# Kernel tuning notes

Hardware: AMD Instinct MI355X
Metric: run time of the kernel (lower is better)

## Reference

```python
import jax, jax.numpy as jnp
import numpy as np

HEAD_DIM = 64
FEAT_H, FEAT_W = 64, 64
ROPE_THETA = 10000.0


def axial_rope_cache(dim, height, width, theta):
    # Matches compute_axial_rope_cache: interleaved cos/sin of shape [H*W, dim]
    theta_dim = (dim // 2) // 2
    freqs = 1.0 / theta ** (jnp.arange(theta_dim, dtype=jnp.float32) * 2.0 / theta_dim)
    t_x = jnp.tile(jnp.arange(width, dtype=jnp.float32)[None, :], (height, 1)).reshape(-1)
    t_y = jnp.tile(jnp.arange(height, dtype=jnp.float32)[:, None], (1, width)).reshape(-1)
    theta_all = jnp.concatenate([jnp.outer(t_x, freqs), jnp.outer(t_y, freqs)], axis=-1)
    cos = jnp.repeat(jnp.cos(theta_all), 2, axis=-1)  # [H*W, dim]
    sin = jnp.repeat(jnp.sin(theta_all), 2, axis=-1)
    return cos, sin


def apply_rope(x, cos, sin):
    # x: [B, H, N, D]; cos/sin: [N, D]
    x1 = x[..., 0::2]
    x2 = x[..., 1::2]
    rot = jnp.stack([-x2, x1], axis=-1).reshape(x.shape)
    return x * cos[None, None] + rot * sin[None, None]


def setup_inputs() -> dict:
    key = jax.random.key(0)
    ks = jax.random.split(key, 11)
    B, Nq, Nk, E, KVD, ID = 1, 4096, 8192, 256, 64, 256
    s_e = 1.0 / np.sqrt(E)
    s_kv = 1.0 / np.sqrt(KVD)
    s_i = 1.0 / np.sqrt(ID)
    return {
        "query": jax.random.normal(ks[0], (B, Nq, E), jnp.float32),
        "key": jax.random.normal(ks[1], (B, Nk, KVD), jnp.float32),
        "value": jax.random.normal(ks[2], (B, Nk, KVD), jnp.float32),
        "Wq": jax.random.normal(ks[3], (E, ID), jnp.float32) * s_e,
        "bq": jnp.zeros((ID,), jnp.float32),
        "Wk": jax.random.normal(ks[4], (KVD, ID), jnp.float32) * s_kv,
        "bk": jnp.zeros((ID,), jnp.float32),
        "Wv": jax.random.normal(ks[5], (KVD, ID), jnp.float32) * s_kv,
        "bv": jnp.zeros((ID,), jnp.float32),
        "Wo": jax.random.normal(ks[6], (ID, E), jnp.float32) * s_i,
        "bo": jnp.zeros((E,), jnp.float32),
        "num_k_exclude_rope": 0,
    }


def reference(query, key, value, Wq, bq, Wk, bk, Wv, bv, Wo, bo, num_k_exclude_rope):
    B, Nq, _ = query.shape
    Nk = key.shape[1]
    H, D = 4, HEAD_DIM

    def split_heads(x):
        b, n, c = x.shape
        return x.reshape(b, n, H, c // H).transpose(0, 2, 1, 3)

    q = split_heads(query @ Wq + bq)  # [B,H,Nq,D]
    k = split_heads(key @ Wk + bk)    # [B,H,Nk,D]
    v = split_heads(value @ Wv + bv)

    cos, sin = axial_rope_cache(D, FEAT_H, FEAT_W, ROPE_THETA)  # [4096, D]
    q = apply_rope(q, cos, sin)

    num_k_rope = Nk - num_k_exclude_rope
    k_spatial = k[:, :, :num_k_rope, :]
    k_other = k[:, :, num_k_rope:, :]
    repeats = num_k_rope // cos.shape[0]  # rope_k_repeat=True
    cos_k = jnp.tile(cos, (repeats, 1))
    sin_k = jnp.tile(sin, (repeats, 1))
    k_spatial = apply_rope(k_spatial, cos_k, sin_k)
    k = jnp.concatenate([k_spatial, k_other], axis=2)

    q = q / jnp.sqrt(jnp.asarray(D, q.dtype))
    scores = jnp.einsum("bhqd,bhkd->bhqk", q, k)
    attn = jax.nn.softmax(scores, axis=-1)
    out = jnp.einsum("bhqk,bhkd->bhqd", attn, v)
    out = out.transpose(0, 2, 1, 3).reshape(B, Nq, H * D)
    return out @ Wo + bo
```

## Files before the change

### kernel.cpp

```cpp
#include <hip/hip_runtime.h>
#include <hip/hip_bf16.h>

#define NQ 4096
#define NK 8192
#define NSPLIT 16
#define KSPAN (NK / NSPLIT)
#define BK 64

#define QSCALE 0.1803368801111204f

typedef short v8s __attribute__((ext_vector_type(8)));
typedef float v4f __attribute__((ext_vector_type(4)));

static __device__ __forceinline__ unsigned short f2bf(float f) {
    unsigned int u = __float_as_uint(f);
    u = (u + 0x7FFFu + ((u >> 16) & 1u)) >> 16;
    return (unsigned short)u;
}
static __device__ __forceinline__ float bf2f(unsigned short h) {
    return __uint_as_float(((unsigned int)h) << 16);
}
static __device__ __forceinline__ unsigned int pkbf(float a, float b) {
    union { __hip_bfloat162 h; unsigned int u; } cv;
    cv.h = __float22bfloat162_rn(make_float2(a, b));
    return cv.u;
}
static __device__ __forceinline__ void split8(const float* a, v8s& hi, v8s& lo) {
#pragma unroll
    for (int j = 0; j < 8; ++j) {
        unsigned short h = f2bf(a[j]);
        hi[j] = (short)h;
        lo[j] = (short)f2bf(a[j] - bf2f(h));
    }
}
static __device__ __forceinline__ void wload(const unsigned short* __restrict__ H,
                                             const unsigned short* __restrict__ L,
                                             int k0, int col, v8s& wh, v8s& wl) {
    const size_t f = (size_t)((k0 >> 3) * 256 + col) * 8;
    wh = *(const v8s*)(H + f);
    wl = *(const v8s*)(L + f);
}
static __device__ __forceinline__ void dma16(const unsigned short* g, unsigned short* l) {
    __builtin_amdgcn_global_load_lds(
        (const __attribute__((address_space(1))) unsigned int*)(const void*)g,
        (__attribute__((address_space(3))) unsigned int*)(void*)l, 16, 0, 0);
}

__global__ __launch_bounds__(256) void prep_kernel(
    const float* __restrict__ Wq, const float* __restrict__ Wk,
    const float* __restrict__ Wv, const float* __restrict__ Wo,
    unsigned short* __restrict__ WqH, unsigned short* __restrict__ WqL,
    unsigned short* __restrict__ WkH, unsigned short* __restrict__ WkL,
    unsigned short* __restrict__ WvH, unsigned short* __restrict__ WvL,
    unsigned short* __restrict__ WoH, unsigned short* __restrict__ WoL)
{
    const int tid = blockIdx.x * 256 + threadIdx.x;
    const float* W;
    unsigned short *H, *L;
    int f;
    if (tid < 8192)        { W = Wq; H = WqH; L = WqL; f = tid; }
    else if (tid < 10240)  { W = Wk; H = WkH; L = WkL; f = tid - 8192; }
    else if (tid < 12288)  { W = Wv; H = WvH; L = WvL; f = tid - 10240; }
    else                   { W = Wo; H = WoH; L = WoL; f = tid - 12288; }
    const int col = f & 255, k0 = (f >> 8) << 3;
    float wv[8];
#pragma unroll
    for (int j = 0; j < 8; ++j) wv[j] = W[(size_t)(k0 + j) * 256 + col];
    v8s hi, lo;
    split8(wv, hi, lo);
    *(v8s*)(H + (size_t)f * 8) = hi;
    *(v8s*)(L + (size_t)f * 8) = lo;
}

__global__ __launch_bounds__(256) void qkv_kernel(
    const float* __restrict__ query, const float* __restrict__ key,
    const float* __restrict__ value,
    const unsigned short* __restrict__ WqH, const unsigned short* __restrict__ WqL,
    const unsigned short* __restrict__ WkH, const unsigned short* __restrict__ WkL,
    const unsigned short* __restrict__ WvH, const unsigned short* __restrict__ WvL,
    const float* __restrict__ bq, const float* __restrict__ bk,
    const float* __restrict__ bv,
    unsigned short* __restrict__ Qb, unsigned short* __restrict__ Kb,
    unsigned short* __restrict__ Vt, const int* __restrict__ nexp)
{
    const int b = blockIdx.x;
    const int t = threadIdx.x, w = t >> 6, lane = t & 63;
    const int quad = lane >> 4, l16 = lane & 15;
    const int colbase = w * 64;

    if (b < 256) {
        const int n0 = b * 16;
        v4f acc[4];
#pragma unroll
        for (int ct = 0; ct < 4; ++ct) {
            const float bb = bq[colbase + ct * 16 + l16];
            acc[ct] = v4f{bb, bb, bb, bb};
        }
        const float* arow = query + (size_t)(n0 + l16) * 256 + quad * 8;
#pragma unroll
        for (int k0 = 0; k0 < 256; k0 += 32) {
            float av[8];
            *(float4*)av = *(const float4*)(arow + k0);
            *(float4*)(av + 4) = *(const float4*)(arow + k0 + 4);
            v8s ah, al;
            split8(av, ah, al);
#pragma unroll
            for (int ct = 0; ct < 4; ++ct) {
                v8s wh, wl;
                wload(WqH, WqL, k0 + quad * 8, colbase + ct * 16 + l16, wh, wl);
                acc[ct] = __builtin_amdgcn_mfma_f32_16x16x32_bf16(al, wh, acc[ct], 0, 0, 0);
                acc[ct] = __builtin_amdgcn_mfma_f32_16x16x32_bf16(ah, wl, acc[ct], 0, 0, 0);
                acc[ct] = __builtin_amdgcn_mfma_f32_16x16x32_bf16(ah, wh, acc[ct], 0, 0, 0);
            }
        }
#pragma unroll
        for (int ct = 0; ct < 4; ++ct) {
            const int d = ct * 16 + l16;
            const int j = d >> 1;
            const float freq = exp2f(-(float)(j & 15) * 1.66096404744368f);
            const bool isx = (j < 16), odd = (d & 1);
#pragma unroll
            for (int r = 0; r < 4; ++r) {
                const int p = n0 + quad * 4 + r;
                const float tpos = isx ? (float)(p & 63) : (float)(p >> 6);
                float sn, cs;
                __sincosf(tpos * freq, &sn, &cs);
                const float x = acc[ct][r];
                const float xp = __shfl_xor(x, 1, 64);
                const float y = odd ? fmaf(x, cs, xp * sn) : fmaf(x, cs, -xp * sn);
                Qb[((size_t)(w * NQ + p) << 6) + d] = f2bf(y * QSCALE);
            }
        }
    } else {
        const bool isK = (b < 768);
        const int n0 = (isK ? (b - 256) : (b - 768)) * 16;
        const float* X = isK ? key : value;
        const unsigned short* WH = isK ? WkH : WvH;
        const unsigned short* WL = isK ? WkL : WvL;
        const float* bias = isK ? bk : bv;
        v4f acc[4];
#pragma unroll
        for (int ct = 0; ct < 4; ++ct) {
            const float bb = bias[colbase + ct * 16 + l16];
            acc[ct] = v4f{bb, bb, bb, bb};
        }
        const float* arow = X + (size_t)(n0 + l16) * 64 + quad * 8;
#pragma unroll
        for (int k0 = 0; k0 < 64; k0 += 32) {
            float av[8];
            *(float4*)av = *(const float4*)(arow + k0);
            *(float4*)(av + 4) = *(const float4*)(arow + k0 + 4);
            v8s ah, al;
            split8(av, ah, al);
#pragma unroll
            for (int ct = 0; ct < 4; ++ct) {
                v8s wh, wl;
                wload(WH, WL, k0 + quad * 8, colbase + ct * 16 + l16, wh, wl);
                acc[ct] = __builtin_amdgcn_mfma_f32_16x16x32_bf16(al, wh, acc[ct], 0, 0, 0);
                acc[ct] = __builtin_amdgcn_mfma_f32_16x16x32_bf16(ah, wl, acc[ct], 0, 0, 0);
                acc[ct] = __builtin_amdgcn_mfma_f32_16x16x32_bf16(ah, wh, acc[ct], 0, 0, 0);
            }
        }
        if (isK) {
            const int nro = NK - *nexp;
#pragma unroll
            for (int ct = 0; ct < 4; ++ct) {
                const int d = ct * 16 + l16;
                const int j = d >> 1;
                const float freq = exp2f(-(float)(j & 15) * 1.66096404744368f);
                const bool isx = (j < 16), odd = (d & 1);
#pragma unroll
                for (int r = 0; r < 4; ++r) {
                    const int p = n0 + quad * 4 + r;
                    const int pc = p & 4095;
                    const float tpos = isx ? (float)(pc & 63) : (float)(pc >> 6);
                    float sn, cs;
                    __sincosf(tpos * freq, &sn, &cs);
                    const float x = acc[ct][r];
                    const float xp = __shfl_xor(x, 1, 64);
                    float y = odd ? fmaf(x, cs, xp * sn) : fmaf(x, cs, -xp * sn);
                    y = (p < nro) ? y : x;
                    Kb[((size_t)(w * NK + p) << 6) + d] = f2bf(y);
                }
            }
        } else {
#pragma unroll
            for (int ct = 0; ct < 4; ++ct) {
                const int col = colbase + ct * 16 + l16;
                uint2 u = make_uint2(pkbf(acc[ct][0], acc[ct][1]),
                                     pkbf(acc[ct][2], acc[ct][3]));
                *(uint2*)(Vt + (size_t)col * NK + n0 + quad * 4) = u;
            }
        }
    }
}

__global__ __launch_bounds__(256) void attn_kernel(
    const unsigned short* __restrict__ Qb, const unsigned short* __restrict__ Kb,
    const unsigned short* __restrict__ Vt, unsigned short* __restrict__ Opart,
    float* __restrict__ Lbuf)
{
    __shared__ alignas(16) unsigned short Kl[2][64 * 64];
    __shared__ alignas(16) unsigned short Vl[2][64 * 64];

    const int blk = blockIdx.x;
    const int s = blk & 15, h = (blk >> 4) & 3, qt = blk >> 6;
    const int t = threadIdx.x;
    const int w = t >> 6, lane = t & 63;
    const int quad = lane >> 4, l16 = lane & 15;

    const int q0 = qt * 128 + w * 32;
    v8s qf[2][2];
#pragma unroll
    for (int g = 0; g < 2; ++g) {
        const unsigned short* qr = Qb + ((size_t)(h * NQ + q0 + g * 16 + l16) << 6) + quad * 8;
        qf[g][0] = *(const v8s*)qr;
        qf[g][1] = *(const v8s*)(qr + 32);
    }

    v4f O[4][2];
#pragma unroll
    for (int dt = 0; dt < 4; ++dt)
#pragma unroll
        for (int g = 0; g < 2; ++g) O[dt][g] = v4f{0.f, 0.f, 0.f, 0.f};
    float psum[2] = {0.f, 0.f};

    const unsigned short* Kbase = Kb + (((size_t)h * NK + s * KSPAN) << 6);
    const unsigned short* Vbase = Vt + (size_t)(h * 64) * NK + s * KSPAN;

    const int srow = lane >> 3;
    const int schunk = (lane & 7) ^ srow;
    const int c0off = ((quad ^ (l16 & 7)) * 8);
    const int c1off = c0off ^ 32;
    int voff[2][2];
#pragma unroll
    for (int tv = 0; tv < 2; ++tv)
#pragma unroll
        for (int h2 = 0; h2 < 2; ++h2)
            voff[tv][h2] = (((4 * tv + 2 * h2 + (quad >> 1)) ^ (l16 & 7)) << 3) + 4 * (quad & 1);

    const int NT = KSPAN / BK;

#pragma unroll
    for (int half = 0; half < 2; ++half) {
        const int r0 = w * 16 + half * 8;
        dma16(Kbase + ((size_t)(r0 + srow) << 6) + schunk * 8, &Kl[0][r0 * 64]);
        dma16(Vbase + (size_t)(r0 + srow) * NK + schunk * 8, &Vl[0][r0 * 64]);
    }

    for (int it = 0; it < NT; ++it) {
        const int cur = it & 1;
        __syncthreads();

        if (it + 1 < NT) {
            const int k1 = (it + 1) * BK;
#pragma unroll
            for (int half = 0; half < 2; ++half) {
                const int r0 = w * 16 + half * 8;
                dma16(Kbase + ((size_t)(k1 + r0 + srow) << 6) + schunk * 8, &Kl[cur ^ 1][r0 * 64]);
                dma16(Vbase + (size_t)(r0 + srow) * NK + k1 + schunk * 8, &Vl[cur ^ 1][r0 * 64]);
            }
        }

        const unsigned short* Klc = &Kl[cur][0];
        const unsigned short* Vlc = &Vl[cur][0];

        v8s pf[2][2];
#pragma unroll
        for (int tt = 0; tt < 4; ++tt) {
            const unsigned short* kr = &Klc[(tt * 16 + l16) * 64];
            const v8s kf0 = *(const v8s*)(kr + c0off);
            const v8s kf1 = *(const v8s*)(kr + c1off);
#pragma unroll
            for (int g = 0; g < 2; ++g) {
                v4f a = v4f{0.f, 0.f, 0.f, 0.f};
                a = __builtin_amdgcn_mfma_f32_16x16x32_bf16(kf0, qf[g][0], a, 0, 0, 0);
                a = __builtin_amdgcn_mfma_f32_16x16x32_bf16(kf1, qf[g][1], a, 0, 0, 0);
                const float e0 = __builtin_amdgcn_exp2f(a[0]);
                const float e1 = __builtin_amdgcn_exp2f(a[1]);
                const float e2 = __builtin_amdgcn_exp2f(a[2]);
                const float e3 = __builtin_amdgcn_exp2f(a[3]);
                psum[g] += (e0 + e1) + (e2 + e3);
                unsigned int* pp = (unsigned int*)&pf[g][tt >> 1];
                pp[(tt & 1) * 2 + 0] = pkbf(e0, e1);
                pp[(tt & 1) * 2 + 1] = pkbf(e2, e3);
            }
        }

#pragma unroll
        for (int dt = 0; dt < 4; ++dt) {
            const unsigned short* vr = &Vlc[(dt * 16 + l16) * 64];
#pragma unroll
            for (int tv = 0; tv < 2; ++tv) {
                union { v8s s; uint2 u[2]; } vv;
                vv.u[0] = *(const uint2*)(vr + voff[tv][0]);
                vv.u[1] = *(const uint2*)(vr + voff[tv][1]);
#pragma unroll
                for (int g = 0; g < 2; ++g)
                    O[dt][g] = __builtin_amdgcn_mfma_f32_16x16x32_bf16(vv.s, pf[g][tv], O[dt][g], 0, 0, 0);
            }
        }
    }

#pragma unroll
    for (int g = 0; g < 2; ++g) {
        float p = psum[g];
        p += __shfl_xor(p, 16, 64);
        p += __shfl_xor(p, 32, 64);
        psum[g] = p;
    }
    unsigned short* Ob = Opart + (size_t)blk * 8192;
#pragma unroll
    for (int g = 0; g < 2; ++g) {
        const int row = w * 32 + g * 16 + l16;
#pragma unroll
        for (int dt = 0; dt < 4; ++dt) {
            uint2 u = make_uint2(pkbf(O[dt][g][0], O[dt][g][1]),
                                 pkbf(O[dt][g][2], O[dt][g][3]));
            *(uint2*)(Ob + row * 64 + dt * 16 + quad * 4) = u;
        }
        if (quad == 0) Lbuf[blk * 128 + row] = psum[g];
    }
}

__global__ __launch_bounds__(512) void oproj_kernel(
    const unsigned short* __restrict__ Opart, const float* __restrict__ Lbuf,
    const unsigned short* __restrict__ WoH, const unsigned short* __restrict__ WoL,
    const float* __restrict__ bo, float* __restrict__ out)
{
    __shared__ alignas(16) unsigned short AH[16][264];
    __shared__ alignas(16) unsigned short AL[16][264];

    const int blk = blockIdx.x;
    const int n0 = blk * 16;
    const int qt = n0 >> 7, rr0 = n0 & 127;
    const int t = threadIdx.x;

    {
        const int row = t >> 5;
        const int d0 = (t & 31) * 8;
        const int h = d0 >> 6, dd0 = d0 & 63;
        const int rr = rr0 + row;
        const int base = qt * 64 + h * 16;
        const unsigned short* op = Opart + (size_t)base * 8192 + rr * 64 + dd0;
        float lsum = 0.f;
        float o[8] = {0.f, 0.f, 0.f, 0.f, 0.f, 0.f, 0.f, 0.f};
#pragma unroll
        for (int s = 0; s < NSPLIT; ++s) {
            lsum += Lbuf[(base + s) * 128 + rr];
            v8s a = *(const v8s*)(op + (size_t)s * 8192);
#pragma unroll
            for (int j = 0; j < 8; ++j) o[j] += bf2f((unsigned short)a[j]);
        }
        const float inv = 1.f / lsum;
#pragma unroll
        for (int j = 0; j < 8; ++j) o[j] *= inv;
        v8s hi, lo;
        split8(o, hi, lo);
        *(v8s*)&AH[row][d0] = hi;
        *(v8s*)&AL[row][d0] = lo;
    }
    __syncthreads();

    const int w = t >> 6, lane = t & 63;
    const int quad = lane >> 4, l16 = lane & 15;
    const int colbase = w * 32;
    v4f acc[2];
#pragma unroll
    for (int ct = 0; ct < 2; ++ct) {
        const float bb = bo[colbase + ct * 16 + l16];
        acc[ct] = v4f{bb, bb, bb, bb};
    }
#pragma unroll
    for (int k0 = 0; k0 < 256; k0 += 32) {
        const v8s ah = *(const v8s*)&AH[l16][k0 + quad * 8];
        const v8s al = *(const v8s*)&AL[l16][k0 + quad * 8];
#pragma unroll
        for (int ct = 0; ct < 2; ++ct) {
            v8s wh, wl;
            wload(WoH, WoL, k0 + quad * 8, colbase + ct * 16 + l16, wh, wl);
            acc[ct] = __builtin_amdgcn_mfma_f32_16x16x32_bf16(al, wh, acc[ct], 0, 0, 0);
            acc[ct] = __builtin_amdgcn_mfma_f32_16x16x32_bf16(ah, wl, acc[ct], 0, 0, 0);
            acc[ct] = __builtin_amdgcn_mfma_f32_16x16x32_bf16(ah, wh, acc[ct], 0, 0, 0);
        }
    }
#pragma unroll
    for (int ct = 0; ct < 2; ++ct)
#pragma unroll
        for (int r = 0; r < 4; ++r)
            out[(size_t)(n0 + quad * 4 + r) * 256 + colbase + ct * 16 + l16] = acc[ct][r];
}

extern "C" void kernel_launch(void* const* d_in, const int* in_sizes, int n_in,
                              void* d_out, int out_size, void* d_ws, size_t ws_size,
                              hipStream_t stream) {
    const float* query = (const float*)d_in[0];
    const float* key   = (const float*)d_in[1];
    const float* value = (const float*)d_in[2];
    const float* Wq    = (const float*)d_in[3];
    const float* bq    = (const float*)d_in[4];
    const float* Wk    = (const float*)d_in[5];
    const float* bk    = (const float*)d_in[6];
    const float* Wv    = (const float*)d_in[7];
    const float* bv    = (const float*)d_in[8];
    const float* Wo    = (const float*)d_in[9];
    const float* bo    = (const float*)d_in[10];
    const int*   nex   = (const int*)d_in[11];

    char* ws = (char*)d_ws;
    const size_t MB = 1024 * 1024;
    unsigned short* Qb    = (unsigned short*)(ws);
    unsigned short* Kb    = (unsigned short*)(ws + 2 * MB);
    unsigned short* Vt    = (unsigned short*)(ws + 6 * MB);
    unsigned short* Opart = (unsigned short*)(ws + 10 * MB);
    float* Lbuf           = (float*)(ws + 42 * MB);
    unsigned short* Wpl   = (unsigned short*)(ws + 43 * MB);
    unsigned short* WqH = Wpl;
    unsigned short* WqL = Wpl + 65536;
    unsigned short* WkH = Wpl + 131072;
    unsigned short* WkL = Wpl + 147456;
    unsigned short* WvH = Wpl + 163840;
    unsigned short* WvL = Wpl + 180224;
    unsigned short* WoH = Wpl + 196608;
    unsigned short* WoL = Wpl + 262144;
    float* out = (float*)d_out;

    prep_kernel<<<80, 256, 0, stream>>>(Wq, Wk, Wv, Wo,
                                        WqH, WqL, WkH, WkL, WvH, WvL, WoH, WoL);
    qkv_kernel<<<1280, 256, 0, stream>>>(query, key, value,
                                         WqH, WqL, WkH, WkL, WvH, WvL,
                                         bq, bk, bv, Qb, Kb, Vt, nex);
    attn_kernel<<<2048, 256, 0, stream>>>(Qb, Kb, Vt, Opart, Lbuf);
    oproj_kernel<<<256, 512, 0, stream>>>(Opart, Lbuf, WoH, WoL, bo, out);
}
```

Baseline: 155.2 us.

## Drop LDS staging in attention, load K/V fragments from global; halve split count

The attention kernel no longer double-buffers K and V tiles into LDS with async global-to-LDS copies and barriers. Each lane now reads its MFMA K and V fragments straight from global memory, relying on L1/L2 caching across the four waves that share them. The key-split count is also halved from 16 to 8, so there are fewer blocks doing longer loops, fewer partial outputs, and a smaller reduction in oproj. The trade is no more barriers and no LDS use, but repeated uncoalesced global reads per wave and less latency hiding with half the blocks.

```diff
diff --git a/kernel.cpp b/kernel.cpp
--- a/kernel.cpp
+++ b/kernel.cpp
@@ -3,7 +3,7 @@
 
 #define NQ 4096
 #define NK 8192
-#define NSPLIT 16
+#define NSPLIT 8
 #define KSPAN (NK / NSPLIT)
 #define BK 64
 
@@ -39,11 +39,6 @@
     const size_t f = (size_t)((k0 >> 3) * 256 + col) * 8;
     wh = *(const v8s*)(H + f);
     wl = *(const v8s*)(L + f);
-}
-static __device__ __forceinline__ void dma16(const unsigned short* g, unsigned short* l) {
-    __builtin_amdgcn_global_load_lds(
-        (const __attribute__((address_space(1))) unsigned int*)(const void*)g,
-        (__attribute__((address_space(3))) unsigned int*)(void*)l, 16, 0, 0);
 }
 
 __global__ __launch_bounds__(256) void prep_kernel(
@@ -200,11 +195,8 @@
     const unsigned short* __restrict__ Vt, unsigned short* __restrict__ Opart,
     float* __restrict__ Lbuf)
 {
-    __shared__ alignas(16) unsigned short Kl[2][64 * 64];
-    __shared__ alignas(16) unsigned short Vl[2][64 * 64];
-
     const int blk = blockIdx.x;
-    const int s = blk & 15, h = (blk >> 4) & 3, qt = blk >> 6;
+    const int s = blk & 7, h = (blk >> 3) & 3, qt = blk >> 5;
     const int t = threadIdx.x;
     const int w = t >> 6, lane = t & 63;
     const int quad = lane >> 4, l16 = lane & 15;
@@ -225,52 +217,16 @@
         for (int g = 0; g < 2; ++g) O[dt][g] = v4f{0.f, 0.f, 0.f, 0.f};
     float psum[2] = {0.f, 0.f};
 
-    const unsigned short* Kbase = Kb + (((size_t)h * NK + s * KSPAN) << 6);
-    const unsigned short* Vbase = Vt + (size_t)(h * 64) * NK + s * KSPAN;
-
-    const int srow = lane >> 3;
-    const int schunk = (lane & 7) ^ srow;
-    const int c0off = ((quad ^ (l16 & 7)) * 8);
-    const int c1off = c0off ^ 32;
-    int voff[2][2];
-#pragma unroll
-    for (int tv = 0; tv < 2; ++tv)
-#pragma unroll
-        for (int h2 = 0; h2 < 2; ++h2)
-            voff[tv][h2] = (((4 * tv + 2 * h2 + (quad >> 1)) ^ (l16 & 7)) << 3) + 4 * (quad & 1);
-
-    const int NT = KSPAN / BK;
-
-#pragma unroll
-    for (int half = 0; half < 2; ++half) {
-        const int r0 = w * 16 + half * 8;
-        dma16(Kbase + ((size_t)(r0 + srow) << 6) + schunk * 8, &Kl[0][r0 * 64]);
-        dma16(Vbase + (size_t)(r0 + srow) * NK + schunk * 8, &Vl[0][r0 * 64]);
-    }
-
-    for (int it = 0; it < NT; ++it) {
-        const int cur = it & 1;
-        __syncthreads();
-
-        if (it + 1 < NT) {
-            const int k1 = (it + 1) * BK;
-#pragma unroll
-            for (int half = 0; half < 2; ++half) {
-                const int r0 = w * 16 + half * 8;
-                dma16(Kbase + ((size_t)(k1 + r0 + srow) << 6) + schunk * 8, &Kl[cur ^ 1][r0 * 64]);
-                dma16(Vbase + (size_t)(r0 + srow) * NK + k1 + schunk * 8, &Vl[cur ^ 1][r0 * 64]);
-            }
-        }
-
-        const unsigned short* Klc = &Kl[cur][0];
-        const unsigned short* Vlc = &Vl[cur][0];
-
+    const unsigned short* Krow = Kb + (((size_t)h * NK + s * KSPAN + l16) << 6) + quad * 8;
+    const unsigned short* Vrow = Vt + (size_t)(h * 64 + l16) * NK + s * KSPAN + quad * 4;
+
+    for (int k0 = 0; k0 < KSPAN; k0 += BK) {
         v8s pf[2][2];
 #pragma unroll
         for (int tt = 0; tt < 4; ++tt) {
-            const unsigned short* kr = &Klc[(tt * 16 + l16) * 64];
-            const v8s kf0 = *(const v8s*)(kr + c0off);
-            const v8s kf1 = *(const v8s*)(kr + c1off);
+            const unsigned short* kr = Krow + ((size_t)(k0 + tt * 16) << 6);
+            const v8s kf0 = *(const v8s*)kr;
+            const v8s kf1 = *(const v8s*)(kr + 32);
 #pragma unroll
             for (int g = 0; g < 2; ++g) {
                 v4f a = v4f{0.f, 0.f, 0.f, 0.f};
@@ -289,12 +245,12 @@
 
 #pragma unroll
         for (int dt = 0; dt < 4; ++dt) {
-            const unsigned short* vr = &Vlc[(dt * 16 + l16) * 64];
+            const unsigned short* vr = Vrow + (size_t)(dt * 16) * NK + k0;
 #pragma unroll
             for (int tv = 0; tv < 2; ++tv) {
                 union { v8s s; uint2 u[2]; } vv;
-                vv.u[0] = *(const uint2*)(vr + voff[tv][0]);
-                vv.u[1] = *(const uint2*)(vr + voff[tv][1]);
+                vv.u[0] = *(const uint2*)(vr + tv * 32);
+                vv.u[1] = *(const uint2*)(vr + tv * 32 + 16);
 #pragma unroll
                 for (int g = 0; g < 2; ++g)
                     O[dt][g] = __builtin_amdgcn_mfma_f32_16x16x32_bf16(vv.s, pf[g][tv], O[dt][g], 0, 0, 0);
@@ -341,7 +297,7 @@
         const int d0 = (t & 31) * 8;
         const int h = d0 >> 6, dd0 = d0 & 63;
         const int rr = rr0 + row;
-        const int base = qt * 64 + h * 16;
+        const int base = qt * 32 + h * 8;
         const unsigned short* op = Opart + (size_t)base * 8192 + rr * 64 + dd0;
         float lsum = 0.f;
         float o[8] = {0.f, 0.f, 0.f, 0.f, 0.f, 0.f, 0.f, 0.f};
@@ -413,8 +369,8 @@
     unsigned short* Kb    = (unsigned short*)(ws + 2 * MB);
     unsigned short* Vt    = (unsigned short*)(ws + 6 * MB);
     unsigned short* Opart = (unsigned short*)(ws + 10 * MB);
-    float* Lbuf           = (float*)(ws + 42 * MB);
-    unsigned short* Wpl   = (unsigned short*)(ws + 43 * MB);
+    float* Lbuf           = (float*)(ws + 26 * MB);
+    unsigned short* Wpl   = (unsigned short*)(ws + 26 * MB + 512 * 1024);
     unsigned short* WqH = Wpl;
     unsigned short* WqL = Wpl + 65536;
     unsigned short* WkH = Wpl + 131072;
@@ -430,6 +386,6 @@
     qkv_kernel<<<1280, 256, 0, stream>>>(query, key, value,
                                          WqH, WqL, WkH, WkL, WvH, WvL,
                                          bq, bk, bv, Qb, Kb, Vt, nex);
-    attn_kernel<<<2048, 256, 0, stream>>>(Qb, Kb, Vt, Opart, Lbuf);
+    attn_kernel<<<1024, 256, 0, stream>>>(Qb, Kb, Vt, Opart, Lbuf);
     oproj_kernel<<<256, 512, 0, stream>>>(Opart, Lbuf, WoH, WoL, bo, out);
 }
```

Result: slower. 280.1 us (+80.5%).
